# Kernel optimization log

Measured on AMD Instinct MI355X. Metric: run time of the kernel, lower is better.

## Reference

```python
import jax, jax.numpy as jnp
import numpy as np

B, N, C0, L = 4, 16, 64, 2048
C1 = C2 = C3 = 128
E = 16384
EPS = 1e-5


def setup_inputs() -> dict:
    key = jax.random.key(0)
    ks = jax.random.split(key, 8)
    x = jax.random.normal(ks[0], (B, N, C0, L), jnp.float32)
    edge_index = jax.random.randint(ks[1], (2, E), 0, L, dtype=jnp.int64)

    def xavier(k, fi, fo):
        s = (2.0 / (fi + fo)) ** 0.5
        return jax.random.normal(k, (fi, fo), jnp.float32) * s

    return dict(
        x=x, edge_index=edge_index,
        W1=xavier(ks[2], C0, C1), b1=jnp.zeros(C1), g1=jnp.ones(C1), be1=jnp.zeros(C1),
        W2=xavier(ks[3], C1, C2), b2=jnp.zeros(C2), g2=jnp.ones(C2), be2=jnp.zeros(C2),
        W3=xavier(ks[4], C2, C3), b3=jnp.zeros(C3), g3=jnp.ones(C3), be3=jnp.zeros(C3),
    )


def _gcn(h, src, dst, norm, self_coef, W, bias):
    # h: [G, L, Cin] -> [G, L, Cout]; improved GCN: A_hat = A + 2I, sym-normalized
    hw = h @ W
    msgs = hw[:, src] * norm[None, :, None]          # [G, E, Cout]
    agg = jnp.zeros_like(hw).at[:, dst].add(msgs)     # scatter-add to targets
    return agg + self_coef[None, :, None] * hw + bias


def _center_bn_relu(h, g, be):
    # h: [G, L, C] -> [G, C, L]; mean-center over set dim n, BatchNorm1d (train), ReLU
    G, Lx, C = h.shape
    z = h.transpose(0, 2, 1).reshape(B, N, C, Lx)
    z = z - z.mean(axis=1, keepdims=True)
    z = z.reshape(G, C, Lx)
    mu = z.mean(axis=(0, 2), keepdims=True)
    var = z.var(axis=(0, 2), keepdims=True)           # biased, matches BN training
    z = (z - mu) / jnp.sqrt(var + EPS) * g[None, :, None] + be[None, :, None]
    return jnp.maximum(z, 0.0)


def reference(x, edge_index, W1, b1, g1, be1, W2, b2, g2, be2, W3, b3, g3, be3):
    b, n, c, l = x.shape
    src, dst = edge_index[0], edge_index[1]
    # improved=True: self-loop weight 2
    deg = jnp.zeros((l,), jnp.float32).at[dst].add(1.0) + 2.0
    dinv = 1.0 / jnp.sqrt(deg)
    norm = dinv[src] * dinv[dst]                      # per-edge coefficient
    self_coef = 2.0 * dinv * dinv                     # per-node self-loop coefficient

    h = x.reshape(b * n, c, l).transpose(0, 2, 1)     # [G, L, C0]

    h = _gcn(h, src, dst, norm, self_coef, W1, b1)
    z = _center_bn_relu(h, g1, be1)                   # [G, C1, L]
    h = z.transpose(0, 2, 1)

    h = _gcn(h, src, dst, norm, self_coef, W2, b2)
    z = _center_bn_relu(h, g2, be2)
    h = z.transpose(0, 2, 1)

    h = _gcn(h, src, dst, norm, self_coef, W3, b3)
    z = _center_bn_relu(h, g3, be3)                   # [G, C3, L]
    return z
```

## Files before the change

### kernel.cpp

```cpp
#include <hip/hip_runtime.h>
#include <hip/hip_bf16.h>

#define GG 64
#define LN 2048
#define BB 4
#define NS 16
#define EE 16384
#define C_0 64
#define CH 128
#define EPSV 1e-5f
#define VK 16
#define GNB 8
#define ECAP 384
#define SLICE ((size_t)LN * 1024)

using bf16x8 = __attribute__((ext_vector_type(8))) short;
using f32x4  = __attribute__((ext_vector_type(4))) float;
using u32x4  = __attribute__((ext_vector_type(4))) unsigned int;
typedef unsigned long long ull;

__device__ __forceinline__ float b2f(unsigned short u) {
    union { unsigned int i; float f; } v; v.i = ((unsigned int)u) << 16; return v.f;
}
__device__ __forceinline__ unsigned short f2b(float f) {
    union { float f; unsigned int i; } v; v.f = f;
    unsigned int r = v.i + 0x7fffu + ((v.i >> 16) & 1u);
    return (unsigned short)(r >> 16);
}
__device__ __forceinline__ void acc8(float* acc, u32x4 v, float w) {
    acc[0] += w * b2f((unsigned short)(v.x & 0xffffu));
    acc[1] += w * b2f((unsigned short)(v.x >> 16));
    acc[2] += w * b2f((unsigned short)(v.y & 0xffffu));
    acc[3] += w * b2f((unsigned short)(v.y >> 16));
    acc[4] += w * b2f((unsigned short)(v.z & 0xffffu));
    acc[5] += w * b2f((unsigned short)(v.z >> 16));
    acc[6] += w * b2f((unsigned short)(v.w & 0xffffu));
    acc[7] += w * b2f((unsigned short)(v.w >> 16));
}
__device__ __forceinline__ void wprep_one(const float* __restrict__ W,
                                          unsigned short* __restrict__ Wp, int idx) {
    int k = idx >> 7, c = idx & (CH - 1);
    int nf = c >> 4, lr = c & 15, ks = k >> 5, hi = (k >> 3) & 3, j = k & 7;
    Wp[(ks * 8 + nf) * 512 + (hi * 16 + lr) * 8 + j] = f2b(W[idx]);
}

__global__ __launch_bounds__(256) void k_prep(
    const int* __restrict__ src, const int* __restrict__ dst,
    const float* __restrict__ W1, const float* __restrict__ W2,
    const float* __restrict__ W3,
    float* __restrict__ selfc, int* __restrict__ off, ull* __restrict__ epack,
    unsigned short* __restrict__ Wp1, unsigned short* __restrict__ Wp2,
    unsigned short* __restrict__ Wp3, float* __restrict__ varK3)
{
    const int bid = blockIdx.x;
    const int t = threadIdx.x;
    if (bid == 0) {
        __shared__ int cntL[LN];
        __shared__ float dinvL[LN];
        __shared__ int offL[LN + 1];
        __shared__ int part[256];
        __shared__ int pre2[256];
        for (int i = t; i < LN; i += 256) cntL[i] = 0;
        __syncthreads();
        for (int e = t; e < EE; e += 256) atomicAdd(&cntL[dst[e]], 1);
        __syncthreads();
        for (int i = t; i < LN; i += 256) {
            float d = (float)cntL[i] + 2.0f;
            float di = rsqrtf(d);
            dinvL[i] = di;
            selfc[i] = 2.0f * di * di;
        }
        {
            const int base = t * 8;
            int loc[8];
            int s = 0;
#pragma unroll
            for (int i = 0; i < 8; i++) { loc[i] = cntL[base + i]; s += loc[i]; }
            part[t] = s;
            __syncthreads();
            if (t == 0) {
                int run = 0;
                for (int i = 0; i < 256; i++) { pre2[i] = run; run += part[i]; }
                offL[LN] = run;
                off[LN] = run;
            }
            __syncthreads();
            int run = pre2[t];
#pragma unroll
            for (int i = 0; i < 8; i++) {
                offL[base + i] = run;
                off[base + i] = run;
                run += loc[i];
            }
        }
        __syncthreads();
        for (int i = t; i < LN; i += 256) cntL[i] = 0;
        __syncthreads();
        for (int e = t; e < EE; e += 256) {
            int s = src[e], d = dst[e];
            int pos = atomicAdd(&cntL[d], 1);
            union { float f; unsigned u; } w;
            w.f = dinvL[s] * dinvL[d];
            epack[offL[d] + pos] = (ull)(unsigned)s | ((ull)w.u << 32);
        }
    } else if (bid == 1) {
        for (int i = t; i < C_0 * CH; i += 256) wprep_one(W1, Wp1, i);
    } else if (bid <= 3) {
        const int base = (bid - 2) * 8192;
        for (int i = t; i < 8192; i += 256) wprep_one(W2, Wp2, base + i);
    } else if (bid <= 5) {
        const int base = (bid - 4) * 8192;
        for (int i = t; i < 8192; i += 256) wprep_one(W3, Wp3, base + i);
    } else {
        for (int i = t; i < 3 * VK * CH; i += 256) varK3[i] = 0.f;
    }
}

template <int K, bool FUSE>
__global__ __launch_bounds__(256) void k_mm(
    const float* __restrict__ X, const unsigned short* __restrict__ Ap,
    const float* __restrict__ varKp, const float* __restrict__ gam,
    const float* __restrict__ bet,
    const unsigned short* __restrict__ Wp, unsigned short* __restrict__ hw)
{
    constexpr int KP = K + 8;
    __shared__ unsigned short As[64 * 136];
    __shared__ float sclL[CH];
    const int g = blockIdx.y;
    const int l0 = blockIdx.x * 64;
    const int t = threadIdx.x;
    const int wq = t >> 6;
    const int lane = t & 63;
    const int lr = lane & 15;
    const int hi = lane >> 4;
    const int kof = hi * 8;

    f32x4 acc[8];
#pragma unroll
    for (int i = 0; i < 8; i++) acc[i] = (f32x4){0.f, 0.f, 0.f, 0.f};

    if (FUSE) {
        if (t < CH) {
            float v = 0.f;
#pragma unroll
            for (int k = 0; k < VK; k++) v += varKp[k * CH + t];
            sclL[t] = gam[t] * rsqrtf(v * (1.f / (GG * LN)) + EPSV);
        }
        __syncthreads();
        const int sg = g >> 5;
        const int gi = g & 31;
        const int row = l0 + wq * 16 + lr;
        bf16x8 aF[K / 32];
#pragma unroll
        for (int ks = 0; ks < K / 32; ks++) {
            const unsigned short* ap = Ap + (size_t)(sg * 4 + ks) * SLICE +
                                       (size_t)row * 1024 + gi * 32 + kof;
            union { uint4 v; unsigned short s[8]; } u;
            u.v = *(const uint4*)ap;
            const int cb = ks * 32 + kof;
            float4 s0 = *(const float4*)&sclL[cb];
            float4 s1 = *(const float4*)&sclL[cb + 4];
            float4 c0 = *(const float4*)&bet[cb];
            float4 c1 = *(const float4*)&bet[cb + 4];
            union { bf16x8 f; unsigned short s[8]; } o;
            o.s[0] = f2b(fmaxf(b2f(u.s[0]) * s0.x + c0.x, 0.f));
            o.s[1] = f2b(fmaxf(b2f(u.s[1]) * s0.y + c0.y, 0.f));
            o.s[2] = f2b(fmaxf(b2f(u.s[2]) * s0.z + c0.z, 0.f));
            o.s[3] = f2b(fmaxf(b2f(u.s[3]) * s0.w + c0.w, 0.f));
            o.s[4] = f2b(fmaxf(b2f(u.s[4]) * s1.x + c1.x, 0.f));
            o.s[5] = f2b(fmaxf(b2f(u.s[5]) * s1.y + c1.y, 0.f));
            o.s[6] = f2b(fmaxf(b2f(u.s[6]) * s1.z + c1.z, 0.f));
            o.s[7] = f2b(fmaxf(b2f(u.s[7]) * s1.w + c1.w, 0.f));
            aF[ks] = o.f;
        }
#pragma unroll
        for (int ks = 0; ks < K / 32; ks++) {
#pragma unroll
            for (int nf = 0; nf < 8; nf++) {
                bf16x8 bF = *(const bf16x8*)&Wp[(ks * 8 + nf) * 512 + lane * 8];
                acc[nf] = __builtin_amdgcn_mfma_f32_16x16x32_bf16(aF[ks], bF,
                                                                  acc[nf], 0, 0, 0);
            }
        }
    } else {
        const int k = t >> 2;
        const int lq = (t & 3) * 16;
        const float* xp = X + ((size_t)g * K + k) * LN + l0 + lq;
#pragma unroll
        for (int i = 0; i < 16; i += 4) {
            float4 v = *(const float4*)&xp[i];
            As[(lq + i + 0) * KP + k] = f2b(v.x);
            As[(lq + i + 1) * KP + k] = f2b(v.y);
            As[(lq + i + 2) * KP + k] = f2b(v.z);
            As[(lq + i + 3) * KP + k] = f2b(v.w);
        }
        __syncthreads();
#pragma unroll
        for (int ks = 0; ks < K / 32; ks++) {
            bf16x8 aF = *(const bf16x8*)&As[(wq * 16 + lr) * KP + ks * 32 + kof];
#pragma unroll
            for (int nf = 0; nf < 8; nf++) {
                bf16x8 bF = *(const bf16x8*)&Wp[(ks * 8 + nf) * 512 + lane * 8];
                acc[nf] = __builtin_amdgcn_mfma_f32_16x16x32_bf16(aF, bF,
                                                                  acc[nf], 0, 0, 0);
            }
        }
        __syncthreads();
    }
#pragma unroll
    for (int nf = 0; nf < 8; nf++) {
#pragma unroll
        for (int r = 0; r < 4; r++) {
            int row = wq * 16 + (lane >> 4) * 4 + r;
            int col = nf * 16 + lr;
            As[row * 136 + col] = f2b(acc[nf][r]);
        }
    }
    __syncthreads();
    {
        const int l = t >> 2;
        const int sc = t & 3;
        unsigned short* hp = hw + (size_t)((g >> 5) * 4 + sc) * SLICE +
                             (size_t)(l0 + l) * 1024 + (g & 31) * 32;
#pragma unroll
        for (int i = 0; i < 32; i += 8)
            *(uint4*)&hp[i] = *(const uint4*)&As[l * 136 + sc * 32 + i];
    }
}

__global__ __launch_bounds__(256) void k_gnv(
    const unsigned short* __restrict__ hw, unsigned short* __restrict__ a,
    float* __restrict__ varK, const int* __restrict__ off,
    const ull* __restrict__ epack, const float* __restrict__ selfc)
{
    __shared__ ull emeta[ECAP];
    __shared__ int soff[GNB + 1];
    __shared__ float sselfc[GNB];
    __shared__ float vred[4][32];
    const int bid = blockIdx.x;
    const int sid = bid & 7;
    const int chunk = bid >> 3;
    const int l0 = chunk * GNB;
    const int t = threadIdx.x;
    const int tr = t >> 7;
    const int ti = t & 127;
    const int lane = t & 63;
    const int wq = t >> 6;
    const int go = ti * 8;
    const unsigned short* hws = hw + sid * SLICE;
    unsigned short* aBs = a + sid * SLICE;

    u32x4 v0s[GNB / 2];
#pragma unroll
    for (int ii = 0; ii < GNB / 2; ii++)
        v0s[ii] = *(const u32x4*)&hws[(size_t)(l0 + ii * 2 + tr) * 1024 + go];

    const int e0 = off[l0];
    const int eTot = off[l0 + GNB] - e0;
    if (t <= GNB) soff[t] = off[l0 + t];
    if (t >= 32 && t < 32 + GNB) sselfc[t - 32] = selfc[l0 + t - 32];
    const int estg = eTot < ECAP ? eTot : ECAP;
    for (int i = t; i < estg; i += 256) emeta[i] = epack[e0 + i];
    __syncthreads();

    float vacc[8] = {0.f, 0.f, 0.f, 0.f, 0.f, 0.f, 0.f, 0.f};

    auto gather = [&](const ull* __restrict__ mp) {
#pragma unroll
        for (int ii = 0; ii < GNB / 2; ii++) {
            const int ln = ii * 2 + tr;
            const int l = l0 + ln;
            const int s0 = soff[ln] - e0;
            const int s1 = soff[ln + 1] - e0;
            const float sc = sselfc[ln];
            float acc[8];
            {
                u32x4 v0 = v0s[ii];
                acc[0] = sc * b2f((unsigned short)(v0.x & 0xffffu));
                acc[1] = sc * b2f((unsigned short)(v0.x >> 16));
                acc[2] = sc * b2f((unsigned short)(v0.y & 0xffffu));
                acc[3] = sc * b2f((unsigned short)(v0.y >> 16));
                acc[4] = sc * b2f((unsigned short)(v0.z & 0xffffu));
                acc[5] = sc * b2f((unsigned short)(v0.z >> 16));
                acc[6] = sc * b2f((unsigned short)(v0.w & 0xffffu));
                acc[7] = sc * b2f((unsigned short)(v0.w >> 16));
            }
            int e = s0;
            for (; e + 4 <= s1; e += 4) {
                ull m0 = mp[e], m1 = mp[e + 1], m2 = mp[e + 2], m3 = mp[e + 3];
                u32x4 vA = *(const u32x4*)&hws[(size_t)(unsigned)m0 * 1024 + go];
                u32x4 vB = *(const u32x4*)&hws[(size_t)(unsigned)m1 * 1024 + go];
                u32x4 vC = *(const u32x4*)&hws[(size_t)(unsigned)m2 * 1024 + go];
                u32x4 vD = *(const u32x4*)&hws[(size_t)(unsigned)m3 * 1024 + go];
                acc8(acc, vA, __uint_as_float((unsigned)(m0 >> 32)));
                acc8(acc, vB, __uint_as_float((unsigned)(m1 >> 32)));
                acc8(acc, vC, __uint_as_float((unsigned)(m2 >> 32)));
                acc8(acc, vD, __uint_as_float((unsigned)(m3 >> 32)));
            }
            for (; e < s1; e++) {
                ull m0 = mp[e];
                u32x4 vA = *(const u32x4*)&hws[(size_t)(unsigned)m0 * 1024 + go];
                acc8(acc, vA, __uint_as_float((unsigned)(m0 >> 32)));
            }
            float m[8];
#pragma unroll
            for (int j = 0; j < 8; j++) m[j] = acc[j];
#pragma unroll
            for (int mask = 4; mask <= 32; mask <<= 1) {
#pragma unroll
                for (int j = 0; j < 8; j++) m[j] += __shfl_xor(m[j], mask);
            }
            u32x4 o;
            unsigned short ob[8];
#pragma unroll
            for (int j = 0; j < 8; j++) {
                float d = acc[j] - m[j] * (1.f / NS);
                vacc[j] += d * d;
                ob[j] = f2b(d);
            }
            o.x = (unsigned int)ob[0] | ((unsigned int)ob[1] << 16);
            o.y = (unsigned int)ob[2] | ((unsigned int)ob[3] << 16);
            o.z = (unsigned int)ob[4] | ((unsigned int)ob[5] << 16);
            o.w = (unsigned int)ob[6] | ((unsigned int)ob[7] << 16);
            __builtin_nontemporal_store(o, (u32x4*)&aBs[(size_t)l * 1024 + go]);
        }
    };
    if (eTot <= ECAP) gather(emeta);
    else gather(epack + e0);

#pragma unroll
    for (int mask = 4; mask <= 32; mask <<= 1) {
#pragma unroll
        for (int j = 0; j < 8; j++) vacc[j] += __shfl_xor(vacc[j], mask);
    }
    if (lane < 4) {
#pragma unroll
        for (int j = 0; j < 8; j++) vred[wq][lane * 8 + j] = vacc[j];
    }
    __syncthreads();
    if (t < 32) {
        float s = vred[0][t] + vred[1][t] + vred[2][t] + vred[3][t];
        atomicAdd(&varK[(chunk & (VK - 1)) * CH + (sid & 3) * 32 + t], s);
    }
}

__global__ __launch_bounds__(256) void k_epi_t(
    const unsigned short* __restrict__ a, const float* __restrict__ varKp,
    const float* __restrict__ gam, const float* __restrict__ bet,
    float* __restrict__ out)
{
    __shared__ unsigned short lds[32 * 16 * 40];
    __shared__ float sclL[CH];
    const int bid = blockIdx.x;
    const int sid = bid & 7;
    const int q = bid >> 3;
    const int gh = q & 1;
    const int chunk = q >> 1;
    const int l0 = chunk * 32;
    const int t = threadIdx.x;
    const int sg = sid >> 2;
    const int sc = sid & 3;
    const unsigned short* aBs = a + sid * SLICE;
    if (t < CH) {
        float v = 0.f;
#pragma unroll
        for (int k = 0; k < VK; k++) v += varKp[k * CH + t];
        sclL[t] = gam[t] * rsqrtf(v * (1.f / (GG * LN)) + EPSV);
    }
    {
        const int qr = t >> 6;
        const int ti = t & 63;
        const int gl = ti >> 2;
        const int c0 = (ti & 3) * 8;
#pragma unroll
        for (int i = 0; i < 8; i++) {
            const int lrow = i * 4 + qr;
            uint4 v = *(const uint4*)&aBs[(size_t)(l0 + lrow) * 1024 + gh * 512 + ti * 8];
            *(uint4*)&lds[(lrow * 16 + gl) * 40 + c0] = v;
        }
    }
    __syncthreads();
#pragma unroll
    for (int it = 0; it < 2; it++) {
        const int p = it * 256 + t;
        const int g2 = p >> 5;
        const int c2 = p & 31;
        const int cG = sc * 32 + c2;
        const int gG = sg * 32 + gh * 16 + g2;
        const float s = sclL[cG], bb = bet[cG];
        float o[32];
#pragma unroll
        for (int l = 0; l < 32; l++)
            o[l] = fmaxf(b2f(lds[(l * 16 + g2) * 40 + c2]) * s + bb, 0.f);
        float* op = &out[((size_t)gG * CH + cG) * LN + l0];
#pragma unroll
        for (int l = 0; l < 32; l += 4)
            *(float4*)&op[l] = make_float4(o[l], o[l + 1], o[l + 2], o[l + 3]);
    }
}

extern "C" void kernel_launch(void* const* d_in, const int* in_sizes, int n_in,
                              void* d_out, int out_size, void* d_ws, size_t ws_size,
                              hipStream_t stream) {
    const float* x   = (const float*)d_in[0];
    const int*   ei  = (const int*)d_in[1];
    const float* W1  = (const float*)d_in[2];
    const float* g1  = (const float*)d_in[4];
    const float* be1 = (const float*)d_in[5];
    const float* W2  = (const float*)d_in[6];
    const float* g2  = (const float*)d_in[8];
    const float* be2 = (const float*)d_in[9];
    const float* W3  = (const float*)d_in[10];
    const float* g3  = (const float*)d_in[12];
    const float* be3 = (const float*)d_in[13];
    const int* srcp = ei;
    const int* dstp = ei + EE;

    char* ws = (char*)d_ws;
    size_t pos = 0;
    auto alloc = [&](size_t bytes) -> void* {
        void* p = ws + pos;
        pos = (pos + bytes + 255) & ~(size_t)255;
        return p;
    };
    const size_t big = (size_t)LN * GG * CH * sizeof(unsigned short);
    unsigned short* aB  = (unsigned short*)alloc(big);
    unsigned short* Wp1 = (unsigned short*)alloc(C_0 * CH * 2);
    unsigned short* Wp2 = (unsigned short*)alloc(CH * CH * 2);
    unsigned short* Wp3 = (unsigned short*)alloc(CH * CH * 2);
    int*   offA  = (int*)alloc((LN + 1) * 4);
    float* selfc = (float*)alloc(LN * 4);
    ull*   epack = (ull*)alloc(EE * 8);
    float* varK3 = (float*)alloc(3 * VK * CH * 4);
    unsigned short* hw = (ws_size >= pos + big) ? (unsigned short*)alloc(big)
                                                : (unsigned short*)d_out;

    k_prep<<<7, 256, 0, stream>>>(srcp, dstp, W1, W2, W3, selfc, offA, epack,
                                  Wp1, Wp2, Wp3, varK3);

    dim3 mmG(LN / 64, GG);
    const int gnvG = (LN / GNB) * 8;
    float* vK1 = varK3;
    float* vK2 = varK3 + VK * CH;
    float* vK3 = varK3 + 2 * VK * CH;

    k_mm<C_0, false><<<mmG, 256, 0, stream>>>(x, nullptr, nullptr, nullptr, nullptr,
                                              Wp1, hw);
    k_gnv<<<gnvG, 256, 0, stream>>>(hw, aB, vK1, offA, epack, selfc);

    k_mm<CH, true><<<mmG, 256, 0, stream>>>(nullptr, aB, vK1, g1, be1, Wp2, hw);
    k_gnv<<<gnvG, 256, 0, stream>>>(hw, aB, vK2, offA, epack, selfc);

    k_mm<CH, true><<<mmG, 256, 0, stream>>>(nullptr, aB, vK2, g2, be2, Wp3, hw);
    k_gnv<<<gnvG, 256, 0, stream>>>(hw, aB, vK3, offA, epack, selfc);

    k_epi_t<<<64 * 2 * 8, 256, 0, stream>>>(aB, vK3, g3, be3, (float*)d_out);
}
```

Baseline: 255.8 us.

## Split single-block CSR graph build into parallel degree, scan and fill kernels

The edge CSR construction (degree count, prefix scan, edge packing) previously ran serially inside one block of the prep kernel, walking all 16384 edges twice with 256 threads. It is now spread across separate kernels: a grid-wide atomic degree count, a one-block scan producing dinv/selfc/offsets, and a grid-wide fill using global atomics. This adds three kernel launches and moves the atomics from shared to global memory, trading launch overhead for parallelism across many CUs.

```diff
diff --git a/kernel.cpp b/kernel.cpp
--- a/kernel.cpp
+++ b/kernel.cpp
@@ -44,65 +44,16 @@
     Wp[(ks * 8 + nf) * 512 + (hi * 16 + lr) * 8 + j] = f2b(W[idx]);
 }
 
-__global__ __launch_bounds__(256) void k_prep(
-    const int* __restrict__ src, const int* __restrict__ dst,
+__global__ __launch_bounds__(256) void k_prep_a(
     const float* __restrict__ W1, const float* __restrict__ W2,
-    const float* __restrict__ W3,
-    float* __restrict__ selfc, int* __restrict__ off, ull* __restrict__ epack,
-    unsigned short* __restrict__ Wp1, unsigned short* __restrict__ Wp2,
-    unsigned short* __restrict__ Wp3, float* __restrict__ varK3)
+    const float* __restrict__ W3, unsigned short* __restrict__ Wp1,
+    unsigned short* __restrict__ Wp2, unsigned short* __restrict__ Wp3,
+    int* __restrict__ cnt, int* __restrict__ cur, float* __restrict__ varK3)
 {
     const int bid = blockIdx.x;
     const int t = threadIdx.x;
     if (bid == 0) {
-        __shared__ int cntL[LN];
-        __shared__ float dinvL[LN];
-        __shared__ int offL[LN + 1];
-        __shared__ int part[256];
-        __shared__ int pre2[256];
-        for (int i = t; i < LN; i += 256) cntL[i] = 0;
-        __syncthreads();
-        for (int e = t; e < EE; e += 256) atomicAdd(&cntL[dst[e]], 1);
-        __syncthreads();
-        for (int i = t; i < LN; i += 256) {
-            float d = (float)cntL[i] + 2.0f;
-            float di = rsqrtf(d);
-            dinvL[i] = di;
-            selfc[i] = 2.0f * di * di;
-        }
-        {
-            const int base = t * 8;
-            int loc[8];
-            int s = 0;
-#pragma unroll
-            for (int i = 0; i < 8; i++) { loc[i] = cntL[base + i]; s += loc[i]; }
-            part[t] = s;
-            __syncthreads();
-            if (t == 0) {
-                int run = 0;
-                for (int i = 0; i < 256; i++) { pre2[i] = run; run += part[i]; }
-                offL[LN] = run;
-                off[LN] = run;
-            }
-            __syncthreads();
-            int run = pre2[t];
-#pragma unroll
-            for (int i = 0; i < 8; i++) {
-                offL[base + i] = run;
-                off[base + i] = run;
-                run += loc[i];
-            }
-        }
-        __syncthreads();
-        for (int i = t; i < LN; i += 256) cntL[i] = 0;
-        __syncthreads();
-        for (int e = t; e < EE; e += 256) {
-            int s = src[e], d = dst[e];
-            int pos = atomicAdd(&cntL[d], 1);
-            union { float f; unsigned u; } w;
-            w.f = dinvL[s] * dinvL[d];
-            epack[offL[d] + pos] = (ull)(unsigned)s | ((ull)w.u << 32);
-        }
+        for (int i = t; i < LN; i += 256) { cnt[i] = 0; cur[i] = 0; }
     } else if (bid == 1) {
         for (int i = t; i < C_0 * CH; i += 256) wprep_one(W1, Wp1, i);
     } else if (bid <= 3) {
@@ -113,6 +64,56 @@
         for (int i = t; i < 8192; i += 256) wprep_one(W3, Wp3, base + i);
     } else {
         for (int i = t; i < 3 * VK * CH; i += 256) varK3[i] = 0.f;
+    }
+}
+
+__global__ void k_deg(const int* __restrict__ dst, int* __restrict__ cnt) {
+    int e = blockIdx.x * blockDim.x + threadIdx.x;
+    if (e < EE) atomicAdd(&cnt[dst[e]], 1);
+}
+
+__global__ __launch_bounds__(256) void k_nscan(
+    const int* __restrict__ cnt, float* __restrict__ dinv,
+    float* __restrict__ selfc, int* __restrict__ off)
+{
+    __shared__ int part[256];
+    __shared__ int pre2[256];
+    const int t = threadIdx.x;
+    const int base = t * 8;
+    int loc[8];
+    int s = 0;
+#pragma unroll
+    for (int i = 0; i < 8; i++) {
+        loc[i] = cnt[base + i];
+        s += loc[i];
+        float d = (float)loc[i] + 2.0f;
+        float di = rsqrtf(d);
+        dinv[base + i] = di;
+        selfc[base + i] = 2.0f * di * di;
+    }
+    part[t] = s;
+    __syncthreads();
+    if (t == 0) {
+        int run = 0;
+        for (int i = 0; i < 256; i++) { pre2[i] = run; run += part[i]; }
+        off[LN] = run;
+    }
+    __syncthreads();
+    int run = pre2[t];
+#pragma unroll
+    for (int i = 0; i < 8; i++) { off[base + i] = run; run += loc[i]; }
+}
+
+__global__ void k_fill(const int* __restrict__ src, const int* __restrict__ dst,
+                       const int* __restrict__ off, int* __restrict__ cur,
+                       const float* __restrict__ dinv, ull* __restrict__ epack) {
+    int e = blockIdx.x * blockDim.x + threadIdx.x;
+    if (e < EE) {
+        int s = src[e], d = dst[e];
+        int pos = atomicAdd(&cur[d], 1);
+        union { float f; unsigned u; } w;
+        w.f = dinv[s] * dinv[d];
+        epack[off[d] + pos] = (ull)(unsigned)s | ((ull)w.u << 32);
     }
 }
 
@@ -428,15 +429,20 @@
     unsigned short* Wp1 = (unsigned short*)alloc(C_0 * CH * 2);
     unsigned short* Wp2 = (unsigned short*)alloc(CH * CH * 2);
     unsigned short* Wp3 = (unsigned short*)alloc(CH * CH * 2);
+    int*   cnt   = (int*)alloc(LN * 4);
+    int*   cur   = (int*)alloc(LN * 4);
     int*   offA  = (int*)alloc((LN + 1) * 4);
+    float* dinv  = (float*)alloc(LN * 4);
     float* selfc = (float*)alloc(LN * 4);
     ull*   epack = (ull*)alloc(EE * 8);
     float* varK3 = (float*)alloc(3 * VK * CH * 4);
     unsigned short* hw = (ws_size >= pos + big) ? (unsigned short*)alloc(big)
                                                 : (unsigned short*)d_out;
 
-    k_prep<<<7, 256, 0, stream>>>(srcp, dstp, W1, W2, W3, selfc, offA, epack,
-                                  Wp1, Wp2, Wp3, varK3);
+    k_prep_a<<<7, 256, 0, stream>>>(W1, W2, W3, Wp1, Wp2, Wp3, cnt, cur, varK3);
+    k_deg<<<EE / 256, 256, 0, stream>>>(dstp, cnt);
+    k_nscan<<<1, 256, 0, stream>>>(cnt, dinv, selfc, offA);
+    k_fill<<<EE / 256, 256, 0, stream>>>(srcp, dstp, offA, cur, dinv, epack);
 
     dim3 mmG(LN / 64, GG);
     const int gnvG = (LN / GNB) * 8;
```

After: 233.8 us. -8.6%, faster.
